# Kernel tuning notes

Hardware: AMD Instinct MI355X
Metric: run time of the kernel (lower is better)

Reference implementation:

```python
import jax, jax.numpy as jnp
import numpy as np

B, NT, NC, EMB = 8, 512, 2048, 512
H, DK, DV = 8, 64, 64
EPS = 1e-6


def setup_inputs() -> dict:
    key = jax.random.key(0)
    ks = jax.random.split(key, 11)
    s = 1.0 / np.sqrt(EMB)
    return {
        "queries": jax.random.normal(ks[0], (B, NT, EMB), jnp.float32),
        "keys": jax.random.normal(ks[1], (B, NC, EMB), jnp.float32),
        "values": jax.random.normal(ks[2], (B, NC, EMB), jnp.float32),
        "W_At": jax.random.normal(ks[3], (H * DK, EMB), jnp.float32) * s,
        "b_At": jax.random.normal(ks[4], (H * DK,), jnp.float32) * s,
        "W_Ac": jax.random.normal(ks[5], (H * DK, EMB), jnp.float32) * s,
        "b_Ac": jax.random.normal(ks[6], (H * DK,), jnp.float32) * s,
        "W_Bc": jax.random.normal(ks[7], (H * DV, EMB), jnp.float32) * s,
        "b_Bc": jax.random.normal(ks[8], (H * DV,), jnp.float32) * s,
        "W_R": jax.random.normal(ks[9], (EMB, H * DV), jnp.float32) * (1.0 / np.sqrt(H * DV)),
        "b_R": jax.random.normal(ks[10], (EMB,), jnp.float32) * (1.0 / np.sqrt(H * DV)),
    }


def reference(queries, keys, values, W_At, b_At, W_Ac, b_Ac, W_Bc, b_Bc, W_R, b_R):
    b_s, n_t, _ = queries.shape
    n_c = keys.shape[1]
    # projections -> (b, h, n, d)
    q = (queries @ W_At.T + b_At).reshape(b_s, n_t, H, DK).transpose(0, 2, 1, 3)
    k = (keys @ W_Ac.T + b_Ac).reshape(b_s, n_c, H, DK).transpose(0, 2, 1, 3)
    v = (values @ W_Bc.T + b_Bc).reshape(b_s, n_c, H, DV).transpose(0, 2, 1, 3)
    # cosine similarity: q.k / max(||q||*||k||, eps) -- no (b,h,nt,nc,dk) broadcast
    dots = jnp.einsum("bhtd,bhcd->bhtc", q, k)
    qn = jnp.linalg.norm(q, axis=-1)  # (b,h,nt)
    kn = jnp.linalg.norm(k, axis=-1)  # (b,h,nc)
    denom = jnp.maximum(qn[..., :, None] * kn[..., None, :], EPS)
    att = jax.nn.softmax(dots / denom, axis=-1)
    out = jnp.einsum("bhtc,bhcd->bhtd", att, v)
    out = out.transpose(0, 2, 1, 3).reshape(b_s, n_t, H * DV)
    out = out @ W_R.T + b_R
    return (out, att)
```

## Files before the change

### kernel.cpp

```cpp
#include <hip/hip_runtime.h>

#define B_   8
#define NT_  512
#define NC_  2048
#define EMB_ 512
#define H_   8

typedef __attribute__((ext_vector_type(8))) short bf16x8;
typedef __attribute__((ext_vector_type(4))) float f32x4;

__device__ __forceinline__ unsigned short f2bf(float x) {
    unsigned u = __float_as_uint(x);
    u += 0x7fffu + ((u >> 16) & 1u);
    return (unsigned short)(u >> 16);
}
__device__ __forceinline__ float b2f(unsigned short h) {
    return __uint_as_float(((unsigned)h) << 16);
}
__device__ __forceinline__ unsigned pkbf(float lo, float hi) {
    unsigned r;
    asm("v_cvt_pk_bf16_f32 %0, %1, %2" : "=v"(r) : "v"(lo), "v"(hi));
    return r;
}

__device__ __forceinline__ int swz(int row, int col) {
    return row * 64 + ((((col >> 3) ^ row) & 7) << 3) + (col & 7);
}

__device__ __forceinline__ bf16x8 ldfrag(const unsigned short* t, int rowbase, int kq) {
    int lane = threadIdx.x & 63;
    int m = rowbase + (lane & 15);
    int k = kq + ((lane >> 4) << 3);
    return *(const bf16x8*)(t + swz(m, k));
}

template<int NCH>
__device__ __forceinline__ void stage_f32(unsigned short* tile, const float* src, int ld) {
    int tid = threadIdx.x;
#pragma unroll
    for (int i = 0; i < NCH; i++) {
        int ch  = tid + i * 256;
        int row = ch >> 3, c8 = ch & 7;
        const float4* p = (const float4*)(src + (size_t)row * ld + c8 * 8);
        float4 a = p[0], b = p[1];
        uint4 u;
        u.x = pkbf(a.x, a.y);
        u.y = pkbf(a.z, a.w);
        u.z = pkbf(b.x, b.y);
        u.w = pkbf(b.z, b.w);
        *(uint4*)(tile + row * 64 + (((c8 ^ row) & 7) << 3)) = u;
    }
}
template<int NCH>
__device__ __forceinline__ void stage_bf(unsigned short* tile, const unsigned short* src, int ld) {
    int tid = threadIdx.x;
#pragma unroll
    for (int i = 0; i < NCH; i++) {
        int ch  = tid + i * 256;
        int row = ch >> 3, c8 = ch & 7;
        uint4 u = *(const uint4*)(src + (size_t)row * ld + c8 * 8);
        *(uint4*)(tile + row * 64 + (((c8 ^ row) & 7) << 3)) = u;
    }
}

__global__ __launch_bounds__(256) void cvtw(const float* w0, const float* w1,
                                            const float* w2, const float* w3,
                                            unsigned short* dst)
{
    int idx = blockIdx.x * 256 + threadIdx.x;
    int m = idx >> 15;
    int off = (idx & 32767) * 8;
    const float* src = m == 0 ? w0 : m == 1 ? w1 : m == 2 ? w2 : w3;
    float4 a = ((const float4*)(src + off))[0];
    float4 b = ((const float4*)(src + off))[1];
    uint4 u;
    u.x = pkbf(a.x, a.y);
    u.y = pkbf(a.z, a.w);
    u.z = pkbf(b.x, b.y);
    u.w = pkbf(b.z, b.w);
    *(uint4*)(dst + (size_t)m * 262144 + off) = u;
}

template<int MODE, bool ABF>
__global__ __launch_bounds__(256, 4) void gemm512(const void* A, const unsigned short* W,
                                                  const float* bias, void* dst, int sh)
{
    __shared__ unsigned short As[64 * 64];
    __shared__ unsigned short Bs[64 * 64];
    int r0 = blockIdx.x * 64;
    int n0 = blockIdx.y * 64;
    int tid = threadIdx.x;
    int w = tid >> 6, quad = (tid >> 4) & 3, l16 = tid & 15;
    f32x4 acc[4] = {};

    for (int k0 = 0; k0 < 512; k0 += 64) {
        __syncthreads();
        if (ABF) stage_bf<2>(As, (const unsigned short*)A + (size_t)r0 * 512 + k0, 512);
        else     stage_f32<2>(As, (const float*)A + (size_t)r0 * 512 + k0, 512);
        stage_bf<2>(Bs, W + (size_t)n0 * 512 + k0, 512);
        __syncthreads();
#pragma unroll
        for (int ks = 0; ks < 2; ks++) {
            bf16x8 af = ldfrag(As, 16 * w, 32 * ks);
#pragma unroll
            for (int nt = 0; nt < 4; nt++) {
                bf16x8 bfr = ldfrag(Bs, 16 * nt, 32 * ks);
                acc[nt] = __builtin_amdgcn_mfma_f32_16x16x32_bf16(af, bfr, acc[nt], 0, 0, 0);
            }
        }
    }

    float vals[4][4];
    float bn[4];
#pragma unroll
    for (int nt = 0; nt < 4; nt++) bn[nt] = bias[n0 + nt * 16 + l16];
#pragma unroll
    for (int nt = 0; nt < 4; nt++)
#pragma unroll
        for (int r = 0; r < 4; r++) vals[nt][r] = acc[nt][r] + bn[nt];

    if (MODE == 0) {
#pragma unroll
        for (int r = 0; r < 4; r++) {
            float ss = 0.f;
#pragma unroll
            for (int nt = 0; nt < 4; nt++) ss += vals[nt][r] * vals[nt][r];
#pragma unroll
            for (int m = 1; m <= 8; m <<= 1) ss += __shfl_xor(ss, m, 64);
            float sc = rsqrtf(fmaxf(ss, 1e-24f));
#pragma unroll
            for (int nt = 0; nt < 4; nt++) vals[nt][r] *= sc;
        }
    }

#pragma unroll
    for (int nt = 0; nt < 4; nt++) {
        int n = n0 + nt * 16 + l16;
        int h = n >> 6, d = n & 63;
#pragma unroll
        for (int r = 0; r < 4; r++) {
            int row = r0 + w * 16 + quad * 4 + r;
            float val = vals[nt][r];
            if (MODE == 0) {
                int b = row >> sh, nloc = row & ((1 << sh) - 1);
                ((unsigned short*)dst)[((((size_t)(b * H_ + h) << sh) + nloc) << 6) + d] = f2bf(val);
            } else if (MODE == 1) {
                int b = row >> sh, nloc = row & ((1 << sh) - 1);
                ((unsigned short*)dst)[(((size_t)((b * H_ + h) * 64 + d)) << sh) + nloc] = f2bf(val);
            } else {
                ((float*)dst)[(size_t)row * 512 + n] = val;
            }
        }
    }
}

__global__ __launch_bounds__(256, 3) void attn_fused(const unsigned short* qh,
                                                     const unsigned short* kh,
                                                     const unsigned short* vt,
                                                     float* attout,
                                                     unsigned short* oh)
{
    __shared__ unsigned short Ks[128 * 64];
    __shared__ unsigned short Vs[2][64 * 64];
    __shared__ unsigned short Pt[2][32 * 64];
    __shared__ float red[4][32];
    __shared__ float invs[32];
    int bh = blockIdx.y;
    int t0 = blockIdx.x * 32;
    int tid = threadIdx.x;
    int w = tid >> 6, quad = (tid >> 4) & 3, l16 = tid & 15;

    stage_bf<1>((unsigned short*)Pt, qh + ((size_t)bh * NT_ + t0) * 64, 64);
    __syncthreads();
    bf16x8 qf[2][2];
#pragma unroll
    for (int mt = 0; mt < 2; mt++)
#pragma unroll
        for (int ks = 0; ks < 2; ks++) qf[mt][ks] = ldfrag((unsigned short*)Pt, 16 * mt, 32 * ks);

    const unsigned short* kbase = kh + (size_t)bh * NC_ * 64;
    const unsigned short* vbase = vt + (size_t)bh * 64 * NC_;

    f32x4 oacc[2] = {};
    float rs[2][4] = {};

    for (int c0 = 0; c0 < NC_; c0 += 128) {
        __syncthreads();
        stage_bf<4>(Ks, kbase + (size_t)c0 * 64, 64);
        stage_bf<2>(Vs[0], vbase + c0, NC_);
        stage_bf<2>(Vs[1], vbase + c0 + 64, NC_);
        __syncthreads();
#pragma unroll
        for (int nt = 0; nt < 2; nt++) {
            int cl = 32 * w + 16 * nt;
            int half = cl >> 6, cc = cl & 63;
#pragma unroll
            for (int mt = 0; mt < 2; mt++) {
                f32x4 acc = {};
#pragma unroll
                for (int ks = 0; ks < 2; ks++) {
                    bf16x8 bfr = ldfrag(Ks, cl, 32 * ks);
                    acc = __builtin_amdgcn_mfma_f32_16x16x32_bf16(qf[mt][ks], bfr, acc, 0, 0, 0);
                }
#pragma unroll
                for (int r = 0; r < 4; r++) {
                    int t = 16 * mt + quad * 4 + r;
                    float p = __expf(acc[r]);
                    rs[mt][r] += p;
                    Pt[half][swz(t, cc + l16)] = f2bf(p);
                }
            }
        }
        __syncthreads();
#pragma unroll
        for (int half = 0; half < 2; half++) {
#pragma unroll
            for (int ks = 0; ks < 2; ks++) {
                bf16x8 vfr = ldfrag(Vs[half], 16 * w, 32 * ks);
#pragma unroll
                for (int mt = 0; mt < 2; mt++) {
                    bf16x8 af = ldfrag((unsigned short*)Pt[half], 16 * mt, 32 * ks);
                    oacc[mt] = __builtin_amdgcn_mfma_f32_16x16x32_bf16(af, vfr, oacc[mt], 0, 0, 0);
                }
            }
        }
    }

#pragma unroll
    for (int mt = 0; mt < 2; mt++)
#pragma unroll
        for (int r = 0; r < 4; r++) {
            float s = rs[mt][r];
#pragma unroll
            for (int m = 1; m <= 8; m <<= 1) s += __shfl_xor(s, m, 64);
            if (l16 == 0) red[w][16 * mt + quad * 4 + r] = s;
        }
    __syncthreads();
    if (tid < 32) invs[tid] = 1.0f / (red[0][tid] + red[1][tid] + red[2][tid] + red[3][tid]);
    __syncthreads();

    {
        int b = bh >> 3, h = bh & 7;
        int d = 16 * w + l16;
#pragma unroll
        for (int mt = 0; mt < 2; mt++)
#pragma unroll
            for (int r = 0; r < 4; r++) {
                int t = 16 * mt + quad * 4 + r;
                oh[(size_t)(b * NT_ + t0 + t) * 512 + h * 64 + d] = f2bf(oacc[mt][r] * invs[t]);
            }
    }

    float* attbase = attout + ((size_t)bh * NT_ + t0) * 2048;
    float myinv[2][4];
#pragma unroll
    for (int mt = 0; mt < 2; mt++)
#pragma unroll
        for (int r = 0; r < 4; r++) myinv[mt][r] = invs[16 * mt + quad * 4 + r];

    for (int c0 = 0; c0 < NC_; c0 += 128) {
        __syncthreads();
        stage_bf<4>(Ks, kbase + (size_t)c0 * 64, 64);
        __syncthreads();
#pragma unroll
        for (int nt = 0; nt < 2; nt++) {
            int cl = 32 * w + 16 * nt;
#pragma unroll
            for (int mt = 0; mt < 2; mt++) {
                f32x4 acc = {};
#pragma unroll
                for (int ks = 0; ks < 2; ks++) {
                    bf16x8 bfr = ldfrag(Ks, cl, 32 * ks);
                    acc = __builtin_amdgcn_mfma_f32_16x16x32_bf16(qf[mt][ks], bfr, acc, 0, 0, 0);
                }
#pragma unroll
                for (int r = 0; r < 4; r++) {
                    int t = 16 * mt + quad * 4 + r;
                    __builtin_nontemporal_store(__expf(acc[r]) * myinv[mt][r],
                                                attbase + (size_t)t * 2048 + c0 + cl + l16);
                }
            }
        }
    }
}

extern "C" void kernel_launch(void* const* d_in, const int* in_sizes, int n_in,
                              void* d_out, int out_size, void* d_ws, size_t ws_size,
                              hipStream_t stream)
{
    (void)in_sizes; (void)n_in; (void)out_size; (void)ws_size;
    const float* queries = (const float*)d_in[0];
    const float* keys    = (const float*)d_in[1];
    const float* values  = (const float*)d_in[2];
    const float* W_At    = (const float*)d_in[3];
    const float* b_At    = (const float*)d_in[4];
    const float* W_Ac    = (const float*)d_in[5];
    const float* b_Ac    = (const float*)d_in[6];
    const float* W_Bc    = (const float*)d_in[7];
    const float* b_Bc    = (const float*)d_in[8];
    const float* W_R     = (const float*)d_in[9];
    const float* b_R     = (const float*)d_in[10];

    float* out0   = (float*)d_out;
    float* attout = out0 + (size_t)B_ * NT_ * EMB_;

    unsigned short* ws = (unsigned short*)d_ws;
    unsigned short* qh = ws;
    unsigned short* kh = qh + (size_t)2097152;
    unsigned short* vt = kh + (size_t)8388608;
    unsigned short* oh = vt + (size_t)8388608;
    unsigned short* wb = oh + (size_t)2097152;

    dim3 blk(256);

    cvtw<<<dim3(512), blk, 0, stream>>>(W_At, W_Ac, W_Bc, W_R, wb);

    gemm512<0, false><<<dim3(4096 / 64, 8),  blk, 0, stream>>>(queries, wb,               b_At, qh, 9);
    gemm512<0, false><<<dim3(16384 / 64, 8), blk, 0, stream>>>(keys,    wb + 262144,      b_Ac, kh, 11);
    gemm512<1, false><<<dim3(16384 / 64, 8), blk, 0, stream>>>(values,  wb + 2 * 262144,  b_Bc, vt, 11);

    attn_fused<<<dim3(NT_ / 32, B_ * H_), blk, 0, stream>>>(qh, kh, vt, attout, oh);

    gemm512<2, true><<<dim3(4096 / 64, 8), blk, 0, stream>>>(oh, wb + 3 * 262144, b_R, out0, 0);
}
```

Baseline: 492.3 us.

## Load MFMA fragments directly from global memory, merge projection launches

Removes LDS staging of the K, V and weight tiles in the GEMMs and in the attention kernel. MFMA fragments are now read straight from global memory, which also drops most barriers. The three input projections are merged into one launch over a z grid dimension. The attention-probability write pass is reworked: operands are swapped so each lane stores an f32x4 vector nontemporally, and the occupancy hint rises from 3 to 4. The cost is redundant global/L2 reads with no LDS reuse, and strided uncoalesced fragment loads, especially for the fp32 activations in the projections.

```diff
diff --git a/kernel.cpp b/kernel.cpp
--- a/kernel.cpp
+++ b/kernel.cpp
@@ -14,9 +14,6 @@
     u += 0x7fffu + ((u >> 16) & 1u);
     return (unsigned short)(u >> 16);
 }
-__device__ __forceinline__ float b2f(unsigned short h) {
-    return __uint_as_float(((unsigned)h) << 16);
-}
 __device__ __forceinline__ unsigned pkbf(float lo, float hi) {
     unsigned r;
     asm("v_cvt_pk_bf16_f32 %0, %1, %2" : "=v"(r) : "v"(lo), "v"(hi));
@@ -34,33 +31,22 @@
     return *(const bf16x8*)(t + swz(m, k));
 }
 
-template<int NCH>
-__device__ __forceinline__ void stage_f32(unsigned short* tile, const float* src, int ld) {
-    int tid = threadIdx.x;
-#pragma unroll
-    for (int i = 0; i < NCH; i++) {
-        int ch  = tid + i * 256;
-        int row = ch >> 3, c8 = ch & 7;
-        const float4* p = (const float4*)(src + (size_t)row * ld + c8 * 8);
-        float4 a = p[0], b = p[1];
-        uint4 u;
-        u.x = pkbf(a.x, a.y);
-        u.y = pkbf(a.z, a.w);
-        u.z = pkbf(b.x, b.y);
-        u.w = pkbf(b.z, b.w);
-        *(uint4*)(tile + row * 64 + (((c8 ^ row) & 7) << 3)) = u;
-    }
-}
-template<int NCH>
-__device__ __forceinline__ void stage_bf(unsigned short* tile, const unsigned short* src, int ld) {
-    int tid = threadIdx.x;
-#pragma unroll
-    for (int i = 0; i < NCH; i++) {
-        int ch  = tid + i * 256;
-        int row = ch >> 3, c8 = ch & 7;
-        uint4 u = *(const uint4*)(src + (size_t)row * ld + c8 * 8);
-        *(uint4*)(tile + row * 64 + (((c8 ^ row) & 7) << 3)) = u;
-    }
+__device__ __forceinline__ bf16x8 gfrag(const unsigned short* base, int rowbase, int ld, int kq) {
+    int lane = threadIdx.x & 63;
+    return *(const bf16x8*)(base + (size_t)(rowbase + (lane & 15)) * ld + kq + (((lane >> 4) & 3) << 3));
+}
+
+__device__ __forceinline__ bf16x8 gfrag_f32(const float* base, int rowbase, int ld, int kq) {
+    int lane = threadIdx.x & 63;
+    const float* p = base + (size_t)(rowbase + (lane & 15)) * ld + kq + (((lane >> 4) & 3) << 3);
+    float4 a = ((const float4*)p)[0];
+    float4 b = ((const float4*)p)[1];
+    union { uint4 u4; bf16x8 h; } cvt;
+    cvt.u4.x = pkbf(a.x, a.y);
+    cvt.u4.y = pkbf(a.z, a.w);
+    cvt.u4.z = pkbf(b.x, b.y);
+    cvt.u4.w = pkbf(b.z, b.w);
+    return cvt.h;
 }
 
 __global__ __launch_bounds__(256) void cvtw(const float* w0, const float* w1,
@@ -81,30 +67,24 @@
     *(uint4*)(dst + (size_t)m * 262144 + off) = u;
 }
 
-template<int MODE, bool ABF>
-__global__ __launch_bounds__(256, 4) void gemm512(const void* A, const unsigned short* W,
-                                                  const float* bias, void* dst, int sh)
-{
-    __shared__ unsigned short As[64 * 64];
-    __shared__ unsigned short Bs[64 * 64];
-    int r0 = blockIdx.x * 64;
-    int n0 = blockIdx.y * 64;
+template<bool ABF>
+__device__ __forceinline__ void gemm_core(const void* A, const unsigned short* W,
+                                          const float* bias, void* dst, int sh, int mode,
+                                          int r0, int n0)
+{
     int tid = threadIdx.x;
     int w = tid >> 6, quad = (tid >> 4) & 3, l16 = tid & 15;
     f32x4 acc[4] = {};
 
+#pragma unroll 2
     for (int k0 = 0; k0 < 512; k0 += 64) {
-        __syncthreads();
-        if (ABF) stage_bf<2>(As, (const unsigned short*)A + (size_t)r0 * 512 + k0, 512);
-        else     stage_f32<2>(As, (const float*)A + (size_t)r0 * 512 + k0, 512);
-        stage_bf<2>(Bs, W + (size_t)n0 * 512 + k0, 512);
-        __syncthreads();
 #pragma unroll
         for (int ks = 0; ks < 2; ks++) {
-            bf16x8 af = ldfrag(As, 16 * w, 32 * ks);
+            bf16x8 af = ABF ? gfrag((const unsigned short*)A, r0 + 16 * w, 512, k0 + 32 * ks)
+                            : gfrag_f32((const float*)A, r0 + 16 * w, 512, k0 + 32 * ks);
 #pragma unroll
             for (int nt = 0; nt < 4; nt++) {
-                bf16x8 bfr = ldfrag(Bs, 16 * nt, 32 * ks);
+                bf16x8 bfr = gfrag(W, n0 + 16 * nt, 512, k0 + 32 * ks);
                 acc[nt] = __builtin_amdgcn_mfma_f32_16x16x32_bf16(af, bfr, acc[nt], 0, 0, 0);
             }
         }
@@ -119,7 +99,7 @@
 #pragma unroll
         for (int r = 0; r < 4; r++) vals[nt][r] = acc[nt][r] + bn[nt];
 
-    if (MODE == 0) {
+    if (mode == 0) {
 #pragma unroll
         for (int r = 0; r < 4; r++) {
             float ss = 0.f;
@@ -141,10 +121,10 @@
         for (int r = 0; r < 4; r++) {
             int row = r0 + w * 16 + quad * 4 + r;
             float val = vals[nt][r];
-            if (MODE == 0) {
+            if (mode == 0) {
                 int b = row >> sh, nloc = row & ((1 << sh) - 1);
                 ((unsigned short*)dst)[((((size_t)(b * H_ + h) << sh) + nloc) << 6) + d] = f2bf(val);
-            } else if (MODE == 1) {
+            } else if (mode == 1) {
                 int b = row >> sh, nloc = row & ((1 << sh) - 1);
                 ((unsigned short*)dst)[(((size_t)((b * H_ + h) * 64 + d)) << sh) + nloc] = f2bf(val);
             } else {
@@ -154,14 +134,35 @@
     }
 }
 
-__global__ __launch_bounds__(256, 3) void attn_fused(const unsigned short* qh,
+__global__ __launch_bounds__(256, 4) void proj3(const float* q, const float* k,
+                                                const float* v, const unsigned short* wb,
+                                                const float* bAt, const float* bAc, const float* bBc,
+                                                unsigned short* qh, unsigned short* kh, unsigned short* vt)
+{
+    int z = blockIdx.z;
+    int r0 = blockIdx.x * 64, n0 = blockIdx.y * 64;
+    if (z == 0) {
+        if (r0 >= 4096) return;
+        gemm_core<false>(q, wb, bAt, qh, 9, 0, r0, n0);
+    } else if (z == 1) {
+        gemm_core<false>(k, wb + 262144, bAc, kh, 11, 0, r0, n0);
+    } else {
+        gemm_core<false>(v, wb + 524288, bBc, vt, 11, 1, r0, n0);
+    }
+}
+
+__global__ __launch_bounds__(256, 4) void outproj(const unsigned short* oh, const unsigned short* wR,
+                                                  const float* bR, float* out0)
+{
+    gemm_core<true>(oh, wR, bR, out0, 0, 2, blockIdx.x * 64, blockIdx.y * 64);
+}
+
+__global__ __launch_bounds__(256, 4) void attn_fused(const unsigned short* qh,
                                                      const unsigned short* kh,
                                                      const unsigned short* vt,
                                                      float* attout,
                                                      unsigned short* oh)
 {
-    __shared__ unsigned short Ks[128 * 64];
-    __shared__ unsigned short Vs[2][64 * 64];
     __shared__ unsigned short Pt[2][32 * 64];
     __shared__ float red[4][32];
     __shared__ float invs[32];
@@ -170,38 +171,31 @@
     int tid = threadIdx.x;
     int w = tid >> 6, quad = (tid >> 4) & 3, l16 = tid & 15;
 
-    stage_bf<1>((unsigned short*)Pt, qh + ((size_t)bh * NT_ + t0) * 64, 64);
-    __syncthreads();
-    bf16x8 qf[2][2];
-#pragma unroll
-    for (int mt = 0; mt < 2; mt++)
-#pragma unroll
-        for (int ks = 0; ks < 2; ks++) qf[mt][ks] = ldfrag((unsigned short*)Pt, 16 * mt, 32 * ks);
-
+    const unsigned short* qbase = qh + ((size_t)bh * NT_ + t0) * 64;
     const unsigned short* kbase = kh + (size_t)bh * NC_ * 64;
     const unsigned short* vbase = vt + (size_t)bh * 64 * NC_;
 
+    bf16x8 qf[2][2];
+#pragma unroll
+    for (int mt = 0; mt < 2; mt++)
+#pragma unroll
+        for (int ks = 0; ks < 2; ks++) qf[mt][ks] = gfrag(qbase, 16 * mt, 64, 32 * ks);
+
     f32x4 oacc[2] = {};
     float rs[2][4] = {};
 
     for (int c0 = 0; c0 < NC_; c0 += 128) {
-        __syncthreads();
-        stage_bf<4>(Ks, kbase + (size_t)c0 * 64, 64);
-        stage_bf<2>(Vs[0], vbase + c0, NC_);
-        stage_bf<2>(Vs[1], vbase + c0 + 64, NC_);
-        __syncthreads();
 #pragma unroll
         for (int nt = 0; nt < 2; nt++) {
             int cl = 32 * w + 16 * nt;
             int half = cl >> 6, cc = cl & 63;
+            bf16x8 kf0 = gfrag(kbase, c0 + cl, 64, 0);
+            bf16x8 kf1 = gfrag(kbase, c0 + cl, 64, 32);
 #pragma unroll
             for (int mt = 0; mt < 2; mt++) {
                 f32x4 acc = {};
-#pragma unroll
-                for (int ks = 0; ks < 2; ks++) {
-                    bf16x8 bfr = ldfrag(Ks, cl, 32 * ks);
-                    acc = __builtin_amdgcn_mfma_f32_16x16x32_bf16(qf[mt][ks], bfr, acc, 0, 0, 0);
-                }
+                acc = __builtin_amdgcn_mfma_f32_16x16x32_bf16(qf[mt][0], kf0, acc, 0, 0, 0);
+                acc = __builtin_amdgcn_mfma_f32_16x16x32_bf16(qf[mt][1], kf1, acc, 0, 0, 0);
 #pragma unroll
                 for (int r = 0; r < 4; r++) {
                     int t = 16 * mt + quad * 4 + r;
@@ -216,7 +210,7 @@
         for (int half = 0; half < 2; half++) {
 #pragma unroll
             for (int ks = 0; ks < 2; ks++) {
-                bf16x8 vfr = ldfrag(Vs[half], 16 * w, 32 * ks);
+                bf16x8 vfr = gfrag(vbase, 16 * w, NC_, c0 + 64 * half + 32 * ks);
 #pragma unroll
                 for (int mt = 0; mt < 2; mt++) {
                     bf16x8 af = ldfrag((unsigned short*)Pt[half], 16 * mt, 32 * ks);
@@ -224,6 +218,7 @@
                 }
             }
         }
+        __syncthreads();
     }
 
 #pragma unroll
@@ -252,33 +247,26 @@
     }
 
     float* attbase = attout + ((size_t)bh * NT_ + t0) * 2048;
-    float myinv[2][4];
-#pragma unroll
-    for (int mt = 0; mt < 2; mt++)
-#pragma unroll
-        for (int r = 0; r < 4; r++) myinv[mt][r] = invs[16 * mt + quad * 4 + r];
-
-    for (int c0 = 0; c0 < NC_; c0 += 128) {
-        __syncthreads();
-        stage_bf<4>(Ks, kbase + (size_t)c0 * 64, 64);
-        __syncthreads();
+    float myinv[2];
+    myinv[0] = invs[l16];
+    myinv[1] = invs[16 + l16];
+
+    for (int c0 = 32 * w; c0 < NC_; c0 += 128) {
 #pragma unroll
         for (int nt = 0; nt < 2; nt++) {
-            int cl = 32 * w + 16 * nt;
+            int cb = c0 + 16 * nt;
+            bf16x8 af0 = gfrag(kbase, cb, 64, 0);
+            bf16x8 af1 = gfrag(kbase, cb, 64, 32);
 #pragma unroll
             for (int mt = 0; mt < 2; mt++) {
                 f32x4 acc = {};
-#pragma unroll
-                for (int ks = 0; ks < 2; ks++) {
-                    bf16x8 bfr = ldfrag(Ks, cl, 32 * ks);
-                    acc = __builtin_amdgcn_mfma_f32_16x16x32_bf16(qf[mt][ks], bfr, acc, 0, 0, 0);
-                }
-#pragma unroll
-                for (int r = 0; r < 4; r++) {
-                    int t = 16 * mt + quad * 4 + r;
-                    __builtin_nontemporal_store(__expf(acc[r]) * myinv[mt][r],
-                                                attbase + (size_t)t * 2048 + c0 + cl + l16);
-                }
+                acc = __builtin_amdgcn_mfma_f32_16x16x32_bf16(af0, qf[mt][0], acc, 0, 0, 0);
+                acc = __builtin_amdgcn_mfma_f32_16x16x32_bf16(af1, qf[mt][1], acc, 0, 0, 0);
+                f32x4 o;
+#pragma unroll
+                for (int r = 0; r < 4; r++) o[r] = __expf(acc[r]) * myinv[mt];
+                __builtin_nontemporal_store(o,
+                    (f32x4*)(attbase + (size_t)(16 * mt + l16) * 2048 + cb + quad * 4));
             }
         }
     }
@@ -305,21 +293,20 @@
     float* attout = out0 + (size_t)B_ * NT_ * EMB_;
 
     unsigned short* ws = (unsigned short*)d_ws;
-    unsigned short* qh = ws;
-    unsigned short* kh = qh + (size_t)2097152;
-    unsigned short* vt = kh + (size_t)8388608;
-    unsigned short* oh = vt + (size_t)8388608;
-    unsigned short* wb = oh + (size_t)2097152;
+    unsigned short* wb = ws;
+    unsigned short* qh = ws + 1048576;
+    unsigned short* kh = ws + 3145728;
+    unsigned short* vt = ws + 11534336;
+    unsigned short* oh = ws + 19922944;
 
     dim3 blk(256);
 
     cvtw<<<dim3(512), blk, 0, stream>>>(W_At, W_Ac, W_Bc, W_R, wb);
 
-    gemm512<0, false><<<dim3(4096 / 64, 8),  blk, 0, stream>>>(queries, wb,               b_At, qh, 9);
-    gemm512<0, false><<<dim3(16384 / 64, 8), blk, 0, stream>>>(keys,    wb + 262144,      b_Ac, kh, 11);
-    gemm512<1, false><<<dim3(16384 / 64, 8), blk, 0, stream>>>(values,  wb + 2 * 262144,  b_Bc, vt, 11);
+    proj3<<<dim3(256, 8, 3), blk, 0, stream>>>(queries, keys, values, wb,
+                                               b_At, b_Ac, b_Bc, qh, kh, vt);
 
     attn_fused<<<dim3(NT_ / 32, B_ * H_), blk, 0, stream>>>(qh, kh, vt, attout, oh);
 
-    gemm512<2, true><<<dim3(4096 / 64, 8), blk, 0, stream>>>(oh, wb + 3 * 262144, b_R, out0, 0);
-}
+    outproj<<<dim3(64, 8), blk, 0, stream>>>(oh, wb + 786432, b_R, out0);
+}
```

Measured after the change: 612.7 us. 1.24x slower.
